# Performance work log

Hardware: AMD Instinct MI355X
Metric: run time of the kernel (lower is better)

The kernel has to match this reference:

```python
import jax, jax.numpy as jnp
import numpy as np

L, P = 16384, 512
DT_MIN, DT_MAX = 0.001, 0.1
THRESHOLD = 1.0  # spike threshold assumed for cartesian_spike


def setup_inputs() -> dict:
    key = jax.random.key(0)
    k1, k2, k3, k4, k5, k6 = jax.random.split(key, 6)
    u = jax.random.normal(k1, (L, P), dtype=jnp.float32)
    # Stored Lambda param: [..., 0] = log(-Re(Lambda)) with Re(Lambda) < 0, [..., 1] = Im(Lambda)
    lam_real_neg = jax.random.uniform(k2, (P,), minval=0.1, maxval=1.0)  # -Re(Lambda)
    lam_imag = jax.random.normal(k3, (P,)) * 3.0
    Lambda = jnp.stack([jnp.log(lam_real_neg), lam_imag], axis=-1).astype(jnp.float32)
    # init_log_steps: log(dt) uniform in [log(dt_min), log(dt_max)], shape (P, 1)
    log_step = (np.log(DT_MIN) + jax.random.uniform(k4, (P, 1)) * (np.log(DT_MAX) - np.log(DT_MIN))).astype(jnp.float32)
    V_re = jax.random.normal(k5, (P, P), dtype=jnp.float32) / np.sqrt(P)
    V_im = jax.random.normal(k6, (P, P), dtype=jnp.float32) / np.sqrt(P)
    return {"u": u, "Lambda": Lambda, "log_step": log_step, "V_re": V_re, "V_im": V_im}


def _binop(q_i, q_j):
    A_i, b_i = q_i
    A_j, b_j = q_j
    return (A_j * A_i, A_j * b_i + b_j)


def reference(u, Lambda, log_step, V_re, V_im):
    # keep_imag = False: u stays real. discretization = 'zoh', activation = 'cartesian_spike'.
    Lambda_tilde = -jnp.exp(Lambda[..., 0]) + 1j * Lambda[..., 1]            # (P,) complex
    step = jnp.exp(log_step[:, 0])                                            # (P,)
    Lambda_bar = jnp.exp(Lambda_tilde * step)                                 # (P,) |.|<1
    # B_tilde = I, so zoh gives B_bar = diag((Lambda_bar - 1)/Lambda); B_bar @ u_t = coef * u_t
    B_coef = (Lambda_bar - 1.0) / Lambda_tilde                                # (P,)
    Lambda_elements = jnp.broadcast_to(Lambda_bar, (u.shape[0], Lambda_bar.shape[0]))
    Bu_elements = B_coef[None, :] * u.astype(Lambda_bar.dtype)                # (L, P) complex
    _, xs = jax.lax.associative_scan(_binop, (Lambda_elements, Bu_elements))  # (L, P)
    V = V_re + 1j * V_im
    xs = xs @ V.T                                                             # vmap(V @ x) over L
    spikes = (xs.real > THRESHOLD).astype(jnp.float32)                        # cartesian_spike
    return spikes
```

## Files before the change

kernel.cpp:

```cpp
#include <hip/hip_runtime.h>

#define L_LEN   16384
#define P_DIM   512
#define CHUNK   128
#define NCHUNK  128

#define KDIM    1024
#define NDIM    512
#define BM      128
#define BN      128
#define BK      64

typedef __bf16 bf16_t;
typedef __bf16 bf16x8 __attribute__((ext_vector_type(8)));
typedef float  floatx4 __attribute__((ext_vector_type(4)));

__device__ __forceinline__ void channel_consts(const float* __restrict__ Lam,
                                               const float* __restrict__ lstep,
                                               int p, float& ar, float& ai,
                                               float& br, float& bi) {
    float lr = -expf(Lam[2 * p + 0]);
    float li = Lam[2 * p + 1];
    float s  = expf(lstep[p]);
    float er = expf(lr * s);
    ar = er * cosf(li * s);
    ai = er * sinf(li * s);
    float dr = ar - 1.0f, di = ai;
    float inv = 1.0f / (lr * lr + li * li);
    br = (dr * lr + di * li) * inv;
    bi = (di * lr - dr * li) * inv;
}

__global__ void __launch_bounds__(P_DIM) k_scan_ends(const float* __restrict__ u,
        const float* __restrict__ Lam, const float* __restrict__ lstep,
        float2* __restrict__ endv) {
    int p = threadIdx.x;
    int c = blockIdx.x;
    float ar, ai, br, bi;
    channel_consts(Lam, lstep, p, ar, ai, br, bi);
    float xr = 0.f, xi = 0.f;
    const float* up = u + (size_t)c * CHUNK * P_DIM + p;
    #pragma unroll 8
    for (int k = 0; k < CHUNK; ++k) {
        float uv = up[(size_t)k * P_DIM];
        float nr = ar * xr - ai * xi + br * uv;
        float ni = ar * xi + ai * xr + bi * uv;
        xr = nr; xi = ni;
    }
    endv[c * P_DIM + p] = make_float2(xr, xi);
}

__global__ void __launch_bounds__(P_DIM) k_carry(const float* __restrict__ Lam,
        const float* __restrict__ lstep, const float2* __restrict__ endv,
        float2* __restrict__ carry) {
    int p = threadIdx.x;
    float lr = -expf(Lam[2 * p + 0]);
    float li = Lam[2 * p + 1];
    float s  = expf(lstep[p]);
    float t  = s * (float)CHUNK;
    float er = expf(lr * t);
    float Ar = er * cosf(li * t);
    float Ai = er * sinf(li * t);
    float xr = 0.f, xi = 0.f;
    #pragma unroll 4
    for (int c = 0; c < NCHUNK; ++c) {
        carry[c * P_DIM + p] = make_float2(xr, xi);
        float2 e = endv[c * P_DIM + p];
        float nr = Ar * xr - Ai * xi + e.x;
        float ni = Ar * xi + Ai * xr + e.y;
        xr = nr; xi = ni;
    }
}

__global__ void __launch_bounds__(P_DIM) k_materialize(const float* __restrict__ u,
        const float* __restrict__ Lam, const float* __restrict__ lstep,
        const float2* __restrict__ carry, bf16_t* __restrict__ A) {
    int p = threadIdx.x;
    int c = blockIdx.x;
    float ar, ai, br, bi;
    channel_consts(Lam, lstep, p, ar, ai, br, bi);
    float2 x0 = carry[c * P_DIM + p];
    float xr = x0.x, xi = x0.y;
    const float* up = u + (size_t)c * CHUNK * P_DIM + p;
    bf16_t* Ap = A + (size_t)c * CHUNK * KDIM;
    #pragma unroll 4
    for (int k = 0; k < CHUNK; ++k) {
        float uv = up[(size_t)k * P_DIM];
        float nr = ar * xr - ai * xi + br * uv;
        float ni = ar * xi + ai * xr + bi * uv;
        xr = nr; xi = ni;
        Ap[(size_t)k * KDIM + p]         = (bf16_t)xr;
        Ap[(size_t)k * KDIM + P_DIM + p] = (bf16_t)xi;
    }
}

__global__ void __launch_bounds__(256) k_bt(const float* __restrict__ Vre,
        const float* __restrict__ Vim, bf16_t* __restrict__ Bt) {
    int idx = blockIdx.x * 256 + threadIdx.x;
    int j = idx >> 10;
    int k = idx & 1023;
    float v = (k < P_DIM) ? Vre[j * P_DIM + k] : -Vim[j * P_DIM + (k - P_DIM)];
    Bt[idx] = (bf16_t)v;
}

__global__ void __launch_bounds__(256) k_gemm(const bf16_t* __restrict__ A,
        const bf16_t* __restrict__ Bt, float* __restrict__ out) {
    __shared__ uint4 As4[BM * BK * 2 / 16];
    __shared__ uint4 Bs4[BN * BK * 2 / 16];

    const int tid  = threadIdx.x;
    const int lane = tid & 63;
    const int w    = tid >> 6;
    const int m0   = blockIdx.x * BM;
    const int n0   = blockIdx.y * BN;
    const int wm   = (w >> 1) * 64;
    const int wn   = (w & 1) * 64;

    const int fr_m = lane & 15;
    const int fr_g = lane >> 4;

    floatx4 acc[4][4];
    #pragma unroll
    for (int i = 0; i < 4; ++i)
        #pragma unroll
        for (int j = 0; j < 4; ++j) {
            floatx4 z = {0.f, 0.f, 0.f, 0.f};
            acc[i][j] = z;
        }

    const bf16_t* Asrc = A  + (size_t)m0 * KDIM;
    const bf16_t* Bsrc = Bt + (size_t)n0 * KDIM;

    for (int kt = 0; kt < KDIM; kt += BK) {
        __syncthreads();
        #pragma unroll
        for (int i = 0; i < 4; ++i) {
            int q   = i * 256 + tid;
            int row = q >> 3;
            int sc  = q & 7;
            int gc  = sc ^ (row & 7);
            As4[q] = *((const uint4*)(Asrc + (size_t)row * KDIM + kt) + gc);
            Bs4[q] = *((const uint4*)(Bsrc + (size_t)row * KDIM + kt) + gc);
        }
        __syncthreads();
        #pragma unroll
        for (int kk = 0; kk < BK; kk += 32) {
            bf16x8 af[4], bf[4];
            #pragma unroll
            for (int i = 0; i < 4; ++i) {
                int m  = wm + i * 16 + fr_m;
                int cc = (kk >> 3) + fr_g;
                int sc = cc ^ (m & 7);
                af[i] = *(const bf16x8*)((const bf16_t*)As4 + m * BK + sc * 8);
            }
            #pragma unroll
            for (int j = 0; j < 4; ++j) {
                int n  = wn + j * 16 + fr_m;
                int cc = (kk >> 3) + fr_g;
                int sc = cc ^ (n & 7);
                bf[j] = *(const bf16x8*)((const bf16_t*)Bs4 + n * BK + sc * 8);
            }
            #pragma unroll
            for (int i = 0; i < 4; ++i)
                #pragma unroll
                for (int j = 0; j < 4; ++j)
                    acc[i][j] = __builtin_amdgcn_mfma_f32_16x16x32_bf16(
                        af[i], bf[j], acc[i][j], 0, 0, 0);
        }
    }

    #pragma unroll
    for (int i = 0; i < 4; ++i)
        #pragma unroll
        for (int j = 0; j < 4; ++j)
            #pragma unroll
            for (int r = 0; r < 4; ++r) {
                int rr = wm + i * 16 + fr_g * 4 + r;
                int cl = wn + j * 16 + fr_m;
                float v = acc[i][j][r];
                out[(size_t)(m0 + rr) * NDIM + (n0 + cl)] = (v > 1.0f) ? 1.0f : 0.0f;
            }
}

extern "C" void kernel_launch(void* const* d_in, const int* in_sizes, int n_in,
                              void* d_out, int out_size, void* d_ws, size_t ws_size,
                              hipStream_t stream) {
    (void)in_sizes; (void)n_in; (void)out_size; (void)ws_size;
    const float* u     = (const float*)d_in[0];
    const float* Lam   = (const float*)d_in[1];
    const float* lstep = (const float*)d_in[2];
    const float* Vre   = (const float*)d_in[3];
    const float* Vim   = (const float*)d_in[4];
    float* out = (float*)d_out;

    char* ws = (char*)d_ws;
    const size_t endv_bytes  = (size_t)NCHUNK * P_DIM * sizeof(float2);
    const size_t carry_bytes = endv_bytes;
    const size_t bt_bytes    = (size_t)NDIM * KDIM * sizeof(bf16_t);
    float2* endv  = (float2*)(ws);
    float2* carry = (float2*)(ws + endv_bytes);
    bf16_t* Bt    = (bf16_t*)(ws + endv_bytes + carry_bytes);
    bf16_t* A     = (bf16_t*)(ws + endv_bytes + carry_bytes + bt_bytes);

    hipLaunchKernelGGL(k_scan_ends, dim3(NCHUNK), dim3(P_DIM), 0, stream,
                       u, Lam, lstep, endv);
    hipLaunchKernelGGL(k_bt, dim3(NDIM * KDIM / 256), dim3(256), 0, stream,
                       Vre, Vim, Bt);
    hipLaunchKernelGGL(k_carry, dim3(1), dim3(P_DIM), 0, stream,
                       Lam, lstep, endv, carry);
    hipLaunchKernelGGL(k_materialize, dim3(NCHUNK), dim3(P_DIM), 0, stream,
                       u, Lam, lstep, carry, A);
    hipLaunchKernelGGL(k_gemm, dim3(L_LEN / BM, NDIM / BN), dim3(256), 0, stream,
                       A, Bt, out);
}
```

Before: 154.2 us.

## Fuse scan materialization into GEMM via shared-memory state tile, shrink chunks

Merges the per-chunk state materialization and the projection GEMM into one kernel. Each block scans a 32-step chunk, writes the interleaved re/im bf16 states into a swizzled shared-memory tile, then multiplies that tile against the full projection matrix, reading B fragments straight from global memory. This removes the global round-trip of the bf16 state matrix and one kernel launch. Chunks shrink to 32 steps, giving 512 chunks for parallelism, which lengthens the serial carry pass. The B matrix now interleaves re and im columns to match the new A layout. Each block rereads all of B through cache with no shared-memory staging, and its M tile is small at 32 rows.

```diff
diff --git a/kernel.cpp b/kernel.cpp
--- a/kernel.cpp
+++ b/kernel.cpp
@@ -2,14 +2,11 @@
 
 #define L_LEN   16384
 #define P_DIM   512
-#define CHUNK   128
-#define NCHUNK  128
+#define CHUNK   32
+#define NCHUNK  512
 
 #define KDIM    1024
 #define NDIM    512
-#define BM      128
-#define BN      128
-#define BK      64
 
 typedef __bf16 bf16_t;
 typedef __bf16 bf16x8 __attribute__((ext_vector_type(8)));
@@ -62,7 +59,7 @@
     float Ar = er * cosf(li * t);
     float Ai = er * sinf(li * t);
     float xr = 0.f, xi = 0.f;
-    #pragma unroll 4
+    #pragma unroll 8
     for (int c = 0; c < NCHUNK; ++c) {
         carry[c * P_DIM + p] = make_float2(xr, xi);
         float2 e = endv[c * P_DIM + p];
@@ -72,113 +69,99 @@
     }
 }
 
-__global__ void __launch_bounds__(P_DIM) k_materialize(const float* __restrict__ u,
-        const float* __restrict__ Lam, const float* __restrict__ lstep,
-        const float2* __restrict__ carry, bf16_t* __restrict__ A) {
-    int p = threadIdx.x;
-    int c = blockIdx.x;
-    float ar, ai, br, bi;
-    channel_consts(Lam, lstep, p, ar, ai, br, bi);
-    float2 x0 = carry[c * P_DIM + p];
-    float xr = x0.x, xi = x0.y;
-    const float* up = u + (size_t)c * CHUNK * P_DIM + p;
-    bf16_t* Ap = A + (size_t)c * CHUNK * KDIM;
-    #pragma unroll 4
-    for (int k = 0; k < CHUNK; ++k) {
-        float uv = up[(size_t)k * P_DIM];
-        float nr = ar * xr - ai * xi + br * uv;
-        float ni = ar * xi + ai * xr + bi * uv;
-        xr = nr; xi = ni;
-        Ap[(size_t)k * KDIM + p]         = (bf16_t)xr;
-        Ap[(size_t)k * KDIM + P_DIM + p] = (bf16_t)xi;
-    }
-}
-
 __global__ void __launch_bounds__(256) k_bt(const float* __restrict__ Vre,
         const float* __restrict__ Vim, bf16_t* __restrict__ Bt) {
     int idx = blockIdx.x * 256 + threadIdx.x;
-    int j = idx >> 10;
-    int k = idx & 1023;
-    float v = (k < P_DIM) ? Vre[j * P_DIM + k] : -Vim[j * P_DIM + (k - P_DIM)];
-    Bt[idx] = (bf16_t)v;
+    int j = idx >> 9;
+    int c = idx & 511;
+    union { unsigned int w; bf16_t h[2]; } pk;
+    pk.h[0] = (bf16_t)Vre[j * P_DIM + c];
+    pk.h[1] = (bf16_t)(-Vim[j * P_DIM + c]);
+    ((unsigned int*)Bt)[idx] = pk.w;
 }
 
-__global__ void __launch_bounds__(256) k_gemm(const bf16_t* __restrict__ A,
-        const bf16_t* __restrict__ Bt, float* __restrict__ out) {
-    __shared__ uint4 As4[BM * BK * 2 / 16];
-    __shared__ uint4 Bs4[BN * BK * 2 / 16];
+__global__ void __launch_bounds__(512, 4) k_fused(const float* __restrict__ u,
+        const float* __restrict__ Lam, const float* __restrict__ lstep,
+        const float2* __restrict__ carry, const bf16_t* __restrict__ Bt,
+        float* __restrict__ out) {
+    __shared__ __align__(16) bf16_t As[CHUNK * KDIM];
 
-    const int tid  = threadIdx.x;
+    const int tid = threadIdx.x;
+    const int c   = blockIdx.x;
+
+    {
+        const int p = tid;
+        float ar, ai, br, bi;
+        channel_consts(Lam, lstep, p, ar, ai, br, bi);
+        float2 x0 = carry[c * P_DIM + p];
+        float xr = x0.x, xi = x0.y;
+        const float* up = u + (size_t)c * CHUNK * P_DIM + p;
+        unsigned int* As32 = (unsigned int*)As;
+        const int scol = p >> 2;
+        const int dwo  = p & 3;
+        #pragma unroll 8
+        for (int t = 0; t < CHUNK; ++t) {
+            float uv = up[(size_t)t * P_DIM];
+            float nr = ar * xr - ai * xi + br * uv;
+            float ni = ar * xi + ai * xr + bi * uv;
+            xr = nr; xi = ni;
+            union { unsigned int w; bf16_t h[2]; } pk;
+            pk.h[0] = (bf16_t)xr;
+            pk.h[1] = (bf16_t)xi;
+            int sc = scol ^ (t & 7);
+            As32[t * (KDIM / 2) + sc * 4 + dwo] = pk.w;
+        }
+    }
+    __syncthreads();
+
     const int lane = tid & 63;
     const int w    = tid >> 6;
-    const int m0   = blockIdx.x * BM;
-    const int n0   = blockIdx.y * BN;
-    const int wm   = (w >> 1) * 64;
-    const int wn   = (w & 1) * 64;
-
     const int fr_m = lane & 15;
     const int fr_g = lane >> 4;
+    const int nb   = w * 64;
 
-    floatx4 acc[4][4];
+    floatx4 acc[2][4];
     #pragma unroll
-    for (int i = 0; i < 4; ++i)
+    for (int i = 0; i < 2; ++i)
         #pragma unroll
         for (int j = 0; j < 4; ++j) {
             floatx4 z = {0.f, 0.f, 0.f, 0.f};
             acc[i][j] = z;
         }
 
-    const bf16_t* Asrc = A  + (size_t)m0 * KDIM;
-    const bf16_t* Bsrc = Bt + (size_t)n0 * KDIM;
-
-    for (int kt = 0; kt < KDIM; kt += BK) {
-        __syncthreads();
+    #pragma unroll 2
+    for (int kk = 0; kk < KDIM; kk += 32) {
+        const int k0 = kk + fr_g * 8;
+        bf16x8 af[2], bfr[4];
         #pragma unroll
-        for (int i = 0; i < 4; ++i) {
-            int q   = i * 256 + tid;
-            int row = q >> 3;
-            int sc  = q & 7;
-            int gc  = sc ^ (row & 7);
-            As4[q] = *((const uint4*)(Asrc + (size_t)row * KDIM + kt) + gc);
-            Bs4[q] = *((const uint4*)(Bsrc + (size_t)row * KDIM + kt) + gc);
+        for (int j = 0; j < 4; ++j) {
+            int n = nb + j * 16 + fr_m;
+            bfr[j] = *(const bf16x8*)(Bt + (size_t)n * KDIM + k0);
         }
-        __syncthreads();
         #pragma unroll
-        for (int kk = 0; kk < BK; kk += 32) {
-            bf16x8 af[4], bf[4];
+        for (int i = 0; i < 2; ++i) {
+            int m  = i * 16 + fr_m;
+            int sc = (k0 >> 3) ^ (m & 7);
+            af[i] = *(const bf16x8*)(As + m * KDIM + sc * 8);
+        }
+        #pragma unroll
+        for (int i = 0; i < 2; ++i)
             #pragma unroll
-            for (int i = 0; i < 4; ++i) {
-                int m  = wm + i * 16 + fr_m;
-                int cc = (kk >> 3) + fr_g;
-                int sc = cc ^ (m & 7);
-                af[i] = *(const bf16x8*)((const bf16_t*)As4 + m * BK + sc * 8);
-            }
-            #pragma unroll
-            for (int j = 0; j < 4; ++j) {
-                int n  = wn + j * 16 + fr_m;
-                int cc = (kk >> 3) + fr_g;
-                int sc = cc ^ (n & 7);
-                bf[j] = *(const bf16x8*)((const bf16_t*)Bs4 + n * BK + sc * 8);
-            }
-            #pragma unroll
-            for (int i = 0; i < 4; ++i)
-                #pragma unroll
-                for (int j = 0; j < 4; ++j)
-                    acc[i][j] = __builtin_amdgcn_mfma_f32_16x16x32_bf16(
-                        af[i], bf[j], acc[i][j], 0, 0, 0);
-        }
+            for (int j = 0; j < 4; ++j)
+                acc[i][j] = __builtin_amdgcn_mfma_f32_16x16x32_bf16(
+                    af[i], bfr[j], acc[i][j], 0, 0, 0);
     }
 
+    float* op = out + (size_t)c * CHUNK * NDIM;
     #pragma unroll
-    for (int i = 0; i < 4; ++i)
+    for (int i = 0; i < 2; ++i)
         #pragma unroll
         for (int j = 0; j < 4; ++j)
             #pragma unroll
             for (int r = 0; r < 4; ++r) {
-                int rr = wm + i * 16 + fr_g * 4 + r;
-                int cl = wn + j * 16 + fr_m;
-                float v = acc[i][j][r];
-                out[(size_t)(m0 + rr) * NDIM + (n0 + cl)] = (v > 1.0f) ? 1.0f : 0.0f;
+                int rr = i * 16 + fr_g * 4 + r;
+                int cl = nb + j * 16 + fr_m;
+                op[(size_t)rr * NDIM + cl] = (acc[i][j][r] > 1.0f) ? 1.0f : 0.0f;
             }
 }
 
@@ -196,20 +179,16 @@
     char* ws = (char*)d_ws;
     const size_t endv_bytes  = (size_t)NCHUNK * P_DIM * sizeof(float2);
     const size_t carry_bytes = endv_bytes;
-    const size_t bt_bytes    = (size_t)NDIM * KDIM * sizeof(bf16_t);
     float2* endv  = (float2*)(ws);
     float2* carry = (float2*)(ws + endv_bytes);
     bf16_t* Bt    = (bf16_t*)(ws + endv_bytes + carry_bytes);
-    bf16_t* A     = (bf16_t*)(ws + endv_bytes + carry_bytes + bt_bytes);
 
     hipLaunchKernelGGL(k_scan_ends, dim3(NCHUNK), dim3(P_DIM), 0, stream,
                        u, Lam, lstep, endv);
-    hipLaunchKernelGGL(k_bt, dim3(NDIM * KDIM / 256), dim3(256), 0, stream,
+    hipLaunchKernelGGL(k_bt, dim3(NDIM * P_DIM / 256), dim3(256), 0, stream,
                        Vre, Vim, Bt);
     hipLaunchKernelGGL(k_carry, dim3(1), dim3(P_DIM), 0, stream,
                        Lam, lstep, endv, carry);
-    hipLaunchKernelGGL(k_materialize, dim3(NCHUNK), dim3(P_DIM), 0, stream,
-                       u, Lam, lstep, carry, A);
-    hipLaunchKernelGGL(k_gemm, dim3(L_LEN / BM, NDIM / BN), dim3(256), 0, stream,
-                       A, Bt, out);
+    hipLaunchKernelGGL(k_fused, dim3(NCHUNK), dim3(512), 0, stream,
+                       u, Lam, lstep, carry, Bt, out);
 }
```

After: 214.6 us. 39.2% more time.
